# Kernel optimization log

Measured on AMD Instinct MI355X. Metric: run time of the kernel, lower is better.

Reference implementation:

```python
import jax, jax.numpy as jnp
from jax import lax
import numpy as np

B, S, H, L = 128, 256, 768, 24


def setup_inputs() -> dict:
    key = jax.random.key(0)
    k_tf, k_len, k_w, k_tr, k_st, k_en = jax.random.split(key, 6)
    token_features = jax.random.normal(k_tf, (B, S, H), dtype=jnp.float32)
    # contiguous valid lengths in [3, S] (>=3 so that stripping CLS/SEP leaves >=1 token)
    lengths = jax.random.randint(k_len, (B,), 3, S + 1)
    pos = jnp.arange(S)
    input_mask = (pos[None, :] < lengths[:, None]).astype(jnp.int32)
    true_label_mask = (pos[None, :] < (lengths - 2)[:, None]).astype(jnp.int32)
    W = jax.random.normal(k_w, (H, L), dtype=jnp.float32) * 0.02
    b = jnp.zeros((L,), dtype=jnp.float32)
    transitions = jax.random.normal(k_tr, (L, L), dtype=jnp.float32) * 0.1
    start_trans = jax.random.normal(k_st, (L,), dtype=jnp.float32) * 0.1
    end_trans = jax.random.normal(k_en, (L,), dtype=jnp.float32) * 0.1
    return {
        "token_features": token_features,
        "input_mask": input_mask,
        "true_label_mask": true_label_mask,
        "W": W,
        "b": b,
        "transitions": transitions,
        "start_trans": start_trans,
        "end_trans": end_trans,
    }


def _compact(x, mask):
    """Vectorized version of the torch per-token copy loop: for each row,
    gather valid tokens (mask==1) preserving order, drop the first and last
    valid token (CLS/SEP), left-pack into a zero tensor."""
    # stable argsort puts valid positions first, in order
    order = jnp.argsort(1 - mask.astype(jnp.int32), axis=1)  # [B,S]
    gathered = jnp.take_along_axis(x, order[:, :, None], axis=1)  # [B,S,H]
    # drop first valid token (shift left by 1), pad a zero row at the end
    shifted = jnp.concatenate([gathered[:, 1:], jnp.zeros_like(gathered[:, :1])], axis=1)
    n_valid = mask.sum(axis=1)  # [B]
    keep = jnp.arange(x.shape[1])[None, :] < (n_valid[:, None] - 2)  # also drops last (SEP)
    return jnp.where(keep[:, :, None], shifted, 0.0)


def _viterbi(emissions, mask, transitions, start_trans, end_trans):
    """Masked Viterbi decode. emissions [B,S,L], mask [B,S] bool."""
    Bn, Sn, Ln = emissions.shape
    lbl = jnp.arange(Ln)
    score0 = start_trans[None, :] + emissions[:, 0]  # [B,L]

    def step(score, xs):
        em_t, m_t = xs  # [B,L], [B]
        cand = score[:, :, None] + transitions[None]  # [B,prev,curr]
        best = cand.max(axis=1) + em_t
        bp = cand.argmax(axis=1)  # [B,L] best prev tag per curr tag
        new_score = jnp.where(m_t[:, None], best, score)
        bp = jnp.where(m_t[:, None], bp, lbl[None, :])  # identity backpointer on pad
        return new_score, bp

    ems = jnp.swapaxes(emissions[:, 1:], 0, 1)  # [S-1,B,L]
    ms = jnp.swapaxes(mask[:, 1:], 0, 1)  # [S-1,B]
    final, bps = lax.scan(step, score0, (ems, ms))
    final = final + end_trans[None, :]
    best_score = final.max(axis=1)  # [B]
    last_tag = final.argmax(axis=1)  # [B]

    def back(tag, bp):  # tag: tag at time t; bp: bp_t -> tag at t-1
        prev = jnp.take_along_axis(bp, tag[:, None], axis=1)[:, 0]
        return prev, tag

    tag0, tags_rest = lax.scan(back, last_tag, bps, reverse=True)  # tags_rest [S-1,B]
    path = jnp.concatenate([tag0[:, None], jnp.swapaxes(tags_rest, 0, 1)], axis=1)  # [B,S]
    return best_score, path


def reference(token_features, input_mask, true_label_mask, W, b, transitions, start_trans, end_trans):
    mask = input_mask.astype(bool)
    wv = _compact(token_features, mask)  # dropout is identity at inference
    emissions = jax.nn.sigmoid(wv @ W + b)  # [B,S,L]
    _, path = _viterbi(emissions, true_label_mask != 0, transitions, start_trans, end_trans)
    return path
```

## Files before the change

kernel.cpp:

```cpp
#include <hip/hip_runtime.h>
#include <math.h>

#define NB 128
#define NS 256
#define NH 768
#define NL 24
#define ASTR 68
#define SCLS 28

__global__ __launch_bounds__(256) void ner_emis(
    const float* __restrict__ tf, const int* __restrict__ tlm,
    const float* __restrict__ W, const float* __restrict__ bias,
    float* __restrict__ E)
{
    const int b    = blockIdx.x >> 3;
    const int tile = (blockIdx.x & 7) << 5;
    const int tid  = threadIdx.x;
    if (tlm[b*NS + tile] == 0) return;

    __shared__ float lds[8*32*25];
    float* As = lds;
    float* Ws = lds + 32*ASTR;
    float* Pr = lds;

    const int tok  = tid & 15;
    const int ksub = tid >> 4;
    const int kk   = ksub << 2;
    const int rot  = ksub & 3;

    float acc0[NL], acc1[NL];
    #pragma unroll
    for (int l = 0; l < NL; ++l) { acc0[l] = 0.f; acc1[l] = 0.f; }

    const float* tfb = tf + (size_t)(b*NS)*NH;

    const int rowA0 = tid >> 4,            c4A0 = tid & 15;
    const int rowA1 = (tid + 256) >> 4,    c4A1 = tid & 15;
    int trow0 = tile + rowA0 + 1; if (trow0 > 255) trow0 = 255;
    int trow1 = tile + rowA1 + 1; if (trow1 > 255) trow1 = 255;
    const float* srcA0 = tfb + (size_t)trow0*NH + (c4A0 << 2);
    const float* srcA1 = tfb + (size_t)trow1*NH + (c4A1 << 2);

    float4 pa0, pa1, pw0, pw1;
    pa0 = *(const float4*)(srcA0);
    pa1 = *(const float4*)(srcA1);
    {
        const float4* wsrc = (const float4*)(W);
        pw0 = wsrc[tid];
        if (tid < 128) pw1 = wsrc[tid + 256];
    }
    {
        float* d0 = As + rowA0*ASTR + (c4A0 << 2);
        d0[0]=pa0.x; d0[1]=pa0.y; d0[2]=pa0.z; d0[3]=pa0.w;
        float* d1 = As + rowA1*ASTR + (c4A1 << 2);
        d1[0]=pa1.x; d1[1]=pa1.y; d1[2]=pa1.z; d1[3]=pa1.w;
        ((float4*)Ws)[tid] = pw0;
        if (tid < 128) ((float4*)Ws)[tid + 256] = pw1;
    }
    __syncthreads();

    for (int kc0 = 0; kc0 < NH; kc0 += 64) {
        const bool more = (kc0 + 64 < NH);
        if (more) {
            pa0 = *(const float4*)(srcA0 + kc0 + 64);
            pa1 = *(const float4*)(srcA1 + kc0 + 64);
            const float4* wsrc = (const float4*)(W + (size_t)(kc0 + 64)*NL);
            pw0 = wsrc[tid];
            if (tid < 128) pw1 = wsrc[tid + 256];
        }

        const float* A0 = As + tok*ASTR + kk;
        const float* A1 = A0 + 16*ASTR;
        const float* Wr = Ws + kk*NL;
        #pragma unroll
        for (int s = 0; s < 4; ++s) {
            const int j = (s + rot) & 3;
            float a0 = A0[j];
            float a1 = A1[j];
            const float4* w4 = (const float4*)(Wr + j*NL);
            float wv[NL];
            #pragma unroll
            for (int i = 0; i < 6; ++i) {
                float4 w = w4[i];
                wv[4*i+0] = w.x; wv[4*i+1] = w.y; wv[4*i+2] = w.z; wv[4*i+3] = w.w;
            }
            #pragma unroll
            for (int l = 0; l < NL; ++l) {
                acc0[l] = fmaf(a0, wv[l], acc0[l]);
                acc1[l] = fmaf(a1, wv[l], acc1[l]);
            }
        }
        __syncthreads();

        if (more) {
            float* d0 = As + rowA0*ASTR + (c4A0 << 2);
            d0[0]=pa0.x; d0[1]=pa0.y; d0[2]=pa0.z; d0[3]=pa0.w;
            float* d1 = As + rowA1*ASTR + (c4A1 << 2);
            d1[0]=pa1.x; d1[1]=pa1.y; d1[2]=pa1.z; d1[3]=pa1.w;
            ((float4*)Ws)[tid] = pw0;
            if (tid < 128) ((float4*)Ws)[tid + 256] = pw1;
            __syncthreads();
        }
    }

    if (ksub >= 8) {
        float* p = Pr + ((ksub-8)*32 + tok)*25;
        float* q = p + 16*25;
        #pragma unroll
        for (int l = 0; l < NL; ++l) { p[l] = acc0[l]; q[l] = acc1[l]; }
    }
    __syncthreads();
    if (ksub < 8) {
        const float* p = Pr + (ksub*32 + tok)*25;
        const float* q = p + 16*25;
        #pragma unroll
        for (int l = 0; l < NL; ++l) { acc0[l] += p[l]; acc1[l] += q[l]; }
    }
    __syncthreads();
    if (ksub < 8) {
        float* p = Pr + (ksub*32 + tok)*25;
        float* q = p + 16*25;
        #pragma unroll
        for (int l = 0; l < NL; ++l) { p[l] = acc0[l]; q[l] = acc1[l]; }
    }
    __syncthreads();

    const int* tm = tlm + b*NS + tile;
    float* Eb = E + (size_t)(b*NS + tile)*NL;
    #pragma unroll
    for (int i = 0; i < 3; ++i) {
        int o = tid + (i << 8);
        int t = o / NL, l = o % NL;
        if (tm[t]) {
            float s = 0.f;
            #pragma unroll
            for (int ks = 0; ks < 8; ++ks)
                s += Pr[(ks*32 + t)*25 + l];
            float x = s + bias[l];
            Eb[t*NL + l] = 1.0f/(1.0f + expf(-x));
        }
    }
}

__global__ __launch_bounds__(256) void ner_viterbi(
    const float* __restrict__ E, const int* __restrict__ tlm,
    const float* __restrict__ trans, const float* __restrict__ st,
    const float* __restrict__ en, int* __restrict__ out)
{
    const int tid = threadIdx.x;
    const int b   = blockIdx.x;
    const int bS  = b*NS;

    __shared__ float Esh[NS*NL];
    __shared__ float scl[NS*SCLS];
    __shared__ float Tt[NL*NL];
    __shared__ float fin[32];
    __shared__ unsigned char tr_s[NL][NS];
    __shared__ int chosen[12];
    __shared__ int nsh, ltag;

    {
        const float4* src = (const float4*)(E + (size_t)bS*NL);
        float4* dst = (float4*)Esh;
        #pragma unroll
        for (int j = 0; j < 6; ++j) dst[tid + (j << 8)] = src[tid + (j << 8)];
    }
    for (int i = tid; i < NL*NL; i += 256) {
        int c = i / NL, p = i % NL;
        Tt[i] = trans[p*NL + c];
    }
    if (tid < 64) {
        int a = tlm[bS+tid] + tlm[bS+tid+64] + tlm[bS+tid+128] + tlm[bS+tid+192];
        #pragma unroll
        for (int off = 32; off > 0; off >>= 1) a += __shfl_down(a, off, 64);
        if (tid == 0) nsh = a;
    }
    __syncthreads();
    const int n = nsh;

    if (tid < 64) {
        const int lane = tid;
        const int h    = lane >> 5;
        const int c    = lane & 31;
        const int cidx = (c < 24) ? c : 23;
        const int coff = (c < 24) ? c : 24;
        const int p0   = h * 12;

        float Tc[12];
        #pragma unroll
        for (int j = 0; j < 12; ++j) Tc[j] = trans[(p0 + j)*NL + cidx];

        int idxv[12];
        #pragma unroll
        for (int j = 0; j < 12; ++j) idxv[j] = (p0 + j) << 2;

        auto bp = [](int idx4, float v) {
            return __int_as_float(__builtin_amdgcn_ds_bpermute(idx4, __float_as_int(v)));
        };

        float sv = st[cidx] + Esh[cidx];
        scl[coff] = sv;

        auto step = [&](int t, float em) {
            float cand[12];
            #pragma unroll
            for (int j = 0; j < 12; ++j)
                cand[j] = bp(idxv[j], sv) + Tc[j];
            float a0 = fmaxf(fmaxf(cand[0], cand[1]),  cand[2]);
            float a1 = fmaxf(fmaxf(cand[3], cand[4]),  cand[5]);
            float a2 = fmaxf(fmaxf(cand[6], cand[7]),  cand[8]);
            float a3 = fmaxf(fmaxf(cand[9], cand[10]), cand[11]);
            float pm = fmaxf(fmaxf(a0, a1), fmaxf(a2, a3));
#if __has_builtin(__builtin_amdgcn_permlane32_swap)
            auto r = __builtin_amdgcn_permlane32_swap(
                         __float_as_int(pm), __float_as_int(pm), false, false);
            float best = fmaxf(__int_as_float(r[0]), __int_as_float(r[1]));
#else
            float best = fmaxf(pm, bp((lane ^ 32) << 2, pm));
#endif
            sv = best + em;
            scl[t*SCLS + coff] = sv;
        };

        int t = 1;
        for (; t + 8 <= n; t += 8) {
            float em[8];
            const float* eb = Esh + t*NL + cidx;
            #pragma unroll
            for (int j = 0; j < 8; ++j) em[j] = eb[j*NL];
            #pragma unroll
            for (int j = 0; j < 8; ++j) step(t + j, em[j]);
        }
        for (; t < n; ++t) step(t, Esh[t*NL + cidx]);
        fin[c] = sv + en[cidx];
    }
    __syncthreads();

    if (tid == 0) {
        float bv = fin[0]; int bt = 0;
        #pragma unroll
        for (int cc = 1; cc < 24; ++cc) { if (fin[cc] > bv) { bv = fin[cc]; bt = cc; } }
        ltag = bt;
    }
    __syncthreads();

    const int K = (n > 1) ? (n - 1 + 9) / 10 : 1;
    if (n > 1 && tid < 240) {
        const int w = tid / 24 + 1, h = tid % 24;
        int tlo = (w-1)*K; if (tlo > n-1) tlo = n-1;
        int thi = w*K;     if (thi > n-1) thi = n-1;
        int cur = h;
        for (int t = thi; t > tlo; --t) {
            const float4* sp = (const float4*)(scl + (t-1)*SCLS);
            const float4* up = (const float4*)(Tt  + cur*NL);
            float cand[24];
            #pragma unroll
            for (int i = 0; i < 6; ++i) {
                float4 s = sp[i], u = up[i];
                cand[4*i+0] = s.x + u.x;
                cand[4*i+1] = s.y + u.y;
                cand[4*i+2] = s.z + u.z;
                cand[4*i+3] = s.w + u.w;
            }
            float best = cand[0]; int arg = 0;
            #pragma unroll
            for (int p = 1; p < 24; ++p) { if (cand[p] > best) { best = cand[p]; arg = p; } }
            tr_s[h][t-1] = (unsigned char)arg;
            cur = arg;
        }
    }
    __syncthreads();

    if (tid == 0) {
        int cur = ltag;
        for (int w = 10; w >= 1; --w) {
            chosen[w] = cur;
            int tlo = (w-1)*K; if (tlo > n-1) tlo = n-1;
            int thi = w*K;     if (thi > n-1) thi = n-1;
            if (thi > tlo) cur = tr_s[cur][tlo];
        }
    }
    __syncthreads();

    {
        const int t = tid;
        int tag;
        if (t >= n-1) tag = ltag;
        else { int w = t / K + 1; tag = tr_s[chosen[w]][t]; }
        out[bS + t] = tag;
    }
}

extern "C" void kernel_launch(void* const* d_in, const int* in_sizes, int n_in,
                              void* d_out, int out_size, void* d_ws, size_t ws_size,
                              hipStream_t stream) {
    const float* tf    = (const float*)d_in[0];
    const int*   tlm   = (const int*)  d_in[2];
    const float* W     = (const float*)d_in[3];
    const float* bias  = (const float*)d_in[4];
    const float* trans = (const float*)d_in[5];
    const float* st    = (const float*)d_in[6];
    const float* en    = (const float*)d_in[7];
    float* E = (float*)d_ws;

    ner_emis<<<dim3(NB*8), dim3(256), 0, stream>>>(tf, tlm, W, bias, E);
    ner_viterbi<<<dim3(NB), dim3(256), 0, stream>>>(E, tlm, trans, st, en, (int*)d_out);
}
```

Before: 199.9 us.

## Restructure emission GEMM to register-streamed rows and use DPP row-rotate in Viterbi

The emission kernel drops LDS staging of the A and W tiles. Each lane now owns one token and each wave handles a quarter of the K range, reading token features straight from global memory with register prefetch. W is read through uniform scalar loads, and the four wave partials are reduced once in LDS. Blocks grow to 64 tokens, so half as many are launched. The Viterbi recurrence replaces twelve ds_bpermute ops per step with DPP row rotates plus one bpermute swap, masking padded predecessors with a large negative constant. This is meant to cut LDS traffic, barriers and per-step latency, at the cost of more registers and uncoalesced per-lane row loads.

Measured after the change: 298.0 us. 1.49x slower.

```diff
diff --git a/kernel.cpp b/kernel.cpp
--- a/kernel.cpp
+++ b/kernel.cpp
@@ -5,7 +5,6 @@
 #define NS 256
 #define NH 768
 #define NL 24
-#define ASTR 68
 #define SCLS 28
 
 __global__ __launch_bounds__(256) void ner_emis(
@@ -13,131 +12,75 @@
     const float* __restrict__ W, const float* __restrict__ bias,
     float* __restrict__ E)
 {
-    const int b    = blockIdx.x >> 3;
-    const int tile = (blockIdx.x & 7) << 5;
+    const int b    = blockIdx.x >> 2;
+    const int tile = (blockIdx.x & 3) << 6;
     const int tid  = threadIdx.x;
     if (tlm[b*NS + tile] == 0) return;
 
-    __shared__ float lds[8*32*25];
-    float* As = lds;
-    float* Ws = lds + 32*ASTR;
-    float* Pr = lds;
-
-    const int tok  = tid & 15;
-    const int ksub = tid >> 4;
-    const int kk   = ksub << 2;
-    const int rot  = ksub & 3;
-
-    float acc0[NL], acc1[NL];
+    __shared__ float Pr[4*64*25];
+
+    const int lane = tid & 63;
+    const int w    = __builtin_amdgcn_readfirstlane(tid >> 6);
+    const int ks   = w * 192;
+
+    int trow = tile + lane + 1;
+    if (trow > 255) trow = 255;
+    const float* srcA = tf + ((size_t)b*NS + trow)*NH + ks;
+
+    float acc[NL];
     #pragma unroll
-    for (int l = 0; l < NL; ++l) { acc0[l] = 0.f; acc1[l] = 0.f; }
-
-    const float* tfb = tf + (size_t)(b*NS)*NH;
-
-    const int rowA0 = tid >> 4,            c4A0 = tid & 15;
-    const int rowA1 = (tid + 256) >> 4,    c4A1 = tid & 15;
-    int trow0 = tile + rowA0 + 1; if (trow0 > 255) trow0 = 255;
-    int trow1 = tile + rowA1 + 1; if (trow1 > 255) trow1 = 255;
-    const float* srcA0 = tfb + (size_t)trow0*NH + (c4A0 << 2);
-    const float* srcA1 = tfb + (size_t)trow1*NH + (c4A1 << 2);
-
-    float4 pa0, pa1, pw0, pw1;
-    pa0 = *(const float4*)(srcA0);
-    pa1 = *(const float4*)(srcA1);
+    for (int l = 0; l < NL; ++l) acc[l] = 0.f;
+
+    auto fma24 = [&](float av, const float* wr) {
+        #pragma unroll
+        for (int l = 0; l < NL; ++l) acc[l] = fmaf(av, wr[l], acc[l]);
+    };
+
+    float4 c0 = *(const float4*)(srcA);
+    float4 c1 = *(const float4*)(srcA + 4);
+    float4 c2 = *(const float4*)(srcA + 8);
+    float4 c3 = *(const float4*)(srcA + 12);
+
+    for (int kg = 0; kg < 12; ++kg) {
+        float4 n0, n1, n2, n3;
+        const bool more = (kg < 11);
+        if (more) {
+            const float* ns = srcA + ((kg + 1) << 4);
+            n0 = *(const float4*)(ns);
+            n1 = *(const float4*)(ns + 4);
+            n2 = *(const float4*)(ns + 8);
+            n3 = *(const float4*)(ns + 12);
+        }
+        const float* wk = W + (size_t)(ks + (kg << 4))*NL;
+        fma24(c0.x, wk);          fma24(c0.y, wk + NL);
+        fma24(c0.z, wk + 2*NL);   fma24(c0.w, wk + 3*NL);
+        fma24(c1.x, wk + 4*NL);   fma24(c1.y, wk + 5*NL);
+        fma24(c1.z, wk + 6*NL);   fma24(c1.w, wk + 7*NL);
+        fma24(c2.x, wk + 8*NL);   fma24(c2.y, wk + 9*NL);
+        fma24(c2.z, wk + 10*NL);  fma24(c2.w, wk + 11*NL);
+        fma24(c3.x, wk + 12*NL);  fma24(c3.y, wk + 13*NL);
+        fma24(c3.z, wk + 14*NL);  fma24(c3.w, wk + 15*NL);
+        if (more) { c0 = n0; c1 = n1; c2 = n2; c3 = n3; }
+    }
+
     {
-        const float4* wsrc = (const float4*)(W);
-        pw0 = wsrc[tid];
-        if (tid < 128) pw1 = wsrc[tid + 256];
-    }
-    {
-        float* d0 = As + rowA0*ASTR + (c4A0 << 2);
-        d0[0]=pa0.x; d0[1]=pa0.y; d0[2]=pa0.z; d0[3]=pa0.w;
-        float* d1 = As + rowA1*ASTR + (c4A1 << 2);
-        d1[0]=pa1.x; d1[1]=pa1.y; d1[2]=pa1.z; d1[3]=pa1.w;
-        ((float4*)Ws)[tid] = pw0;
-        if (tid < 128) ((float4*)Ws)[tid + 256] = pw1;
-    }
-    __syncthreads();
-
-    for (int kc0 = 0; kc0 < NH; kc0 += 64) {
-        const bool more = (kc0 + 64 < NH);
-        if (more) {
-            pa0 = *(const float4*)(srcA0 + kc0 + 64);
-            pa1 = *(const float4*)(srcA1 + kc0 + 64);
-            const float4* wsrc = (const float4*)(W + (size_t)(kc0 + 64)*NL);
-            pw0 = wsrc[tid];
-            if (tid < 128) pw1 = wsrc[tid + 256];
-        }
-
-        const float* A0 = As + tok*ASTR + kk;
-        const float* A1 = A0 + 16*ASTR;
-        const float* Wr = Ws + kk*NL;
-        #pragma unroll
-        for (int s = 0; s < 4; ++s) {
-            const int j = (s + rot) & 3;
-            float a0 = A0[j];
-            float a1 = A1[j];
-            const float4* w4 = (const float4*)(Wr + j*NL);
-            float wv[NL];
-            #pragma unroll
-            for (int i = 0; i < 6; ++i) {
-                float4 w = w4[i];
-                wv[4*i+0] = w.x; wv[4*i+1] = w.y; wv[4*i+2] = w.z; wv[4*i+3] = w.w;
-            }
-            #pragma unroll
-            for (int l = 0; l < NL; ++l) {
-                acc0[l] = fmaf(a0, wv[l], acc0[l]);
-                acc1[l] = fmaf(a1, wv[l], acc1[l]);
-            }
-        }
-        __syncthreads();
-
-        if (more) {
-            float* d0 = As + rowA0*ASTR + (c4A0 << 2);
-            d0[0]=pa0.x; d0[1]=pa0.y; d0[2]=pa0.z; d0[3]=pa0.w;
-            float* d1 = As + rowA1*ASTR + (c4A1 << 2);
-            d1[0]=pa1.x; d1[1]=pa1.y; d1[2]=pa1.z; d1[3]=pa1.w;
-            ((float4*)Ws)[tid] = pw0;
-            if (tid < 128) ((float4*)Ws)[tid + 256] = pw1;
-            __syncthreads();
-        }
-    }
-
-    if (ksub >= 8) {
-        float* p = Pr + ((ksub-8)*32 + tok)*25;
-        float* q = p + 16*25;
-        #pragma unroll
-        for (int l = 0; l < NL; ++l) { p[l] = acc0[l]; q[l] = acc1[l]; }
-    }
-    __syncthreads();
-    if (ksub < 8) {
-        const float* p = Pr + (ksub*32 + tok)*25;
-        const float* q = p + 16*25;
-        #pragma unroll
-        for (int l = 0; l < NL; ++l) { acc0[l] += p[l]; acc1[l] += q[l]; }
-    }
-    __syncthreads();
-    if (ksub < 8) {
-        float* p = Pr + (ksub*32 + tok)*25;
-        float* q = p + 16*25;
-        #pragma unroll
-        for (int l = 0; l < NL; ++l) { p[l] = acc0[l]; q[l] = acc1[l]; }
+        float* p = Pr + ((w << 6) + lane)*25;
+        #pragma unroll
+        for (int l = 0; l < NL; ++l) p[l] = acc[l];
     }
     __syncthreads();
 
     const int* tm = tlm + b*NS + tile;
     float* Eb = E + (size_t)(b*NS + tile)*NL;
     #pragma unroll
-    for (int i = 0; i < 3; ++i) {
+    for (int i = 0; i < 6; ++i) {
         int o = tid + (i << 8);
-        int t = o / NL, l = o % NL;
+        int t = o / NL, l = o - t*NL;
         if (tm[t]) {
-            float s = 0.f;
-            #pragma unroll
-            for (int ks = 0; ks < 8; ++ks)
-                s += Pr[(ks*32 + t)*25 + l];
+            float s = ((Pr[t*25 + l] + Pr[(64 + t)*25 + l])
+                       + Pr[(128 + t)*25 + l]) + Pr[(192 + t)*25 + l];
             float x = s + bias[l];
-            Eb[t*NL + l] = 1.0f/(1.0f + expf(-x));
+            Eb[o] = 1.0f/(1.0f + expf(-x));
         }
     }
 }
@@ -180,45 +123,55 @@
 
     if (tid < 64) {
         const int lane = tid;
-        const int h    = lane >> 5;
         const int c    = lane & 31;
         const int cidx = (c < 24) ? c : 23;
         const int coff = (c < 24) ? c : 24;
-        const int p0   = h * 12;
-
-        float Tc[12];
-        #pragma unroll
-        for (int j = 0; j < 12; ++j) Tc[j] = trans[(p0 + j)*NL + cidx];
-
-        int idxv[12];
-        #pragma unroll
-        for (int j = 0; j < 12; ++j) idxv[j] = (p0 + j) << 2;
-
-        auto bp = [](int idx4, float v) {
-            return __int_as_float(__builtin_amdgcn_ds_bpermute(idx4, __float_as_int(v)));
-        };
+        const int swIdx = (lane ^ 16) << 2;
+
+        float TA[16], TB[16];
+        {
+            int aP = c;
+            int bP = (lane ^ 16) & 31;
+            TA[0] = (c < 24 && aP < 24) ? trans[aP*NL + cidx] : -1e30f;
+            TB[0] = (c < 24 && bP < 24) ? trans[bP*NL + cidx] : -1e30f;
+        }
+        #define CAL(r) { \
+            int srcl = __builtin_amdgcn_update_dpp(lane, lane, (0x120 + r), 0xF, 0xF, false); \
+            int aP = srcl & 31; int bP = (srcl ^ 16) & 31; \
+            TA[r] = (c < 24 && aP < 24) ? trans[aP*NL + cidx] : -1e30f; \
+            TB[r] = (c < 24 && bP < 24) ? trans[bP*NL + cidx] : -1e30f; }
+        CAL(1)  CAL(2)  CAL(3)  CAL(4)  CAL(5)  CAL(6)  CAL(7)
+        CAL(8)  CAL(9)  CAL(10) CAL(11) CAL(12) CAL(13) CAL(14) CAL(15)
+        #undef CAL
 
         float sv = st[cidx] + Esh[cidx];
         scl[coff] = sv;
 
+        #define F3(x,y,z) fmaxf(fmaxf(x,y),z)
+
         auto step = [&](int t, float em) {
-            float cand[12];
-            #pragma unroll
-            for (int j = 0; j < 12; ++j)
-                cand[j] = bp(idxv[j], sv) + Tc[j];
-            float a0 = fmaxf(fmaxf(cand[0], cand[1]),  cand[2]);
-            float a1 = fmaxf(fmaxf(cand[3], cand[4]),  cand[5]);
-            float a2 = fmaxf(fmaxf(cand[6], cand[7]),  cand[8]);
-            float a3 = fmaxf(fmaxf(cand[9], cand[10]), cand[11]);
-            float pm = fmaxf(fmaxf(a0, a1), fmaxf(a2, a3));
-#if __has_builtin(__builtin_amdgcn_permlane32_swap)
-            auto r = __builtin_amdgcn_permlane32_swap(
-                         __float_as_int(pm), __float_as_int(pm), false, false);
-            float best = fmaxf(__int_as_float(r[0]), __int_as_float(r[1]));
-#else
-            float best = fmaxf(pm, bp((lane ^ 32) << 2, pm));
-#endif
-            sv = best + em;
+            int svi = __float_as_int(sv);
+            int swi = __builtin_amdgcn_ds_bpermute(swIdx, svi);
+            float aa0 = sv + TA[0];
+            #define CA(r) float aa##r = __int_as_float(__builtin_amdgcn_update_dpp( \
+                svi, svi, (0x120 + r), 0xF, 0xF, false)) + TA[r];
+            CA(1)  CA(2)  CA(3)  CA(4)  CA(5)  CA(6)  CA(7)
+            CA(8)  CA(9)  CA(10) CA(11) CA(12) CA(13) CA(14) CA(15)
+            #undef CA
+            float mA = fmaxf(fmaxf(F3(aa0,aa1,aa2),  F3(aa3,aa4,aa5)),
+                       fmaxf(F3(aa6,aa7,aa8),
+                       fmaxf(F3(aa9,aa10,aa11), fmaxf(F3(aa12,aa13,aa14), aa15))));
+            float sswap = __int_as_float(swi);
+            float bb0 = sswap + TB[0];
+            #define CB(r) float bb##r = __int_as_float(__builtin_amdgcn_update_dpp( \
+                swi, swi, (0x120 + r), 0xF, 0xF, false)) + TB[r];
+            CB(1)  CB(2)  CB(3)  CB(4)  CB(5)  CB(6)  CB(7)
+            CB(8)  CB(9)  CB(10) CB(11) CB(12) CB(13) CB(14) CB(15)
+            #undef CB
+            float mB = fmaxf(fmaxf(F3(bb0,bb1,bb2),  F3(bb3,bb4,bb5)),
+                       fmaxf(F3(bb6,bb7,bb8),
+                       fmaxf(F3(bb9,bb10,bb11), fmaxf(F3(bb12,bb13,bb14), bb15))));
+            sv = fmaxf(mA, mB) + em;
             scl[t*SCLS + coff] = sv;
         };
 
@@ -303,6 +256,6 @@
     const float* en    = (const float*)d_in[7];
     float* E = (float*)d_ws;
 
-    ner_emis<<<dim3(NB*8), dim3(256), 0, stream>>>(tf, tlm, W, bias, E);
+    ner_emis<<<dim3(NB*4), dim3(256), 0, stream>>>(tf, tlm, W, bias, E);
     ner_viterbi<<<dim3(NB), dim3(256), 0, stream>>>(E, tlm, trans, st, en, (int*)d_out);
 }
```

## Fuse emission GEMM and Viterbi into one kernel with per-tile flag handoff

Applied to the files above, without the earlier changes.

Merges the emission projection kernel and the Viterbi kernel into a single launch. The first NB blocks run Viterbi and spin on per-tile release flags written by the emission blocks, so each decode chunk starts as soon as its 32-token tile is ready instead of waiting for a full kernel boundary. Emissions are read directly from global memory in 32-step chunks rather than staged into LDS. This removes the launch gap and lets the Viterbi recursion overlap with the GEMM. The cost is an extra memset launch and spinning blocks that hold compute units, and forward progress depends on the emission blocks being scheduled while the Viterbi blocks wait.

After: 252.1 us. +26.1%, slower.

```diff
diff --git a/kernel.cpp b/kernel.cpp
--- a/kernel.cpp
+++ b/kernel.cpp
@@ -7,176 +7,178 @@
 #define NL 24
 #define ASTR 68
 #define SCLS 28
-
-__global__ __launch_bounds__(256) void ner_emis(
+#define E_BYTES (NB*NS*NL*4)
+
+__global__ __launch_bounds__(256) void ner_fused(
     const float* __restrict__ tf, const int* __restrict__ tlm,
     const float* __restrict__ W, const float* __restrict__ bias,
-    float* __restrict__ E)
+    const float* __restrict__ trans, const float* __restrict__ st,
+    const float* __restrict__ en, float* __restrict__ E,
+    int* __restrict__ flags, int* __restrict__ out)
 {
-    const int b    = blockIdx.x >> 3;
-    const int tile = (blockIdx.x & 7) << 5;
-    const int tid  = threadIdx.x;
-    if (tlm[b*NS + tile] == 0) return;
-
-    __shared__ float lds[8*32*25];
-    float* As = lds;
-    float* Ws = lds + 32*ASTR;
-    float* Pr = lds;
-
-    const int tok  = tid & 15;
-    const int ksub = tid >> 4;
-    const int kk   = ksub << 2;
-    const int rot  = ksub & 3;
-
-    float acc0[NL], acc1[NL];
-    #pragma unroll
-    for (int l = 0; l < NL; ++l) { acc0[l] = 0.f; acc1[l] = 0.f; }
-
-    const float* tfb = tf + (size_t)(b*NS)*NH;
-
-    const int rowA0 = tid >> 4,            c4A0 = tid & 15;
-    const int rowA1 = (tid + 256) >> 4,    c4A1 = tid & 15;
-    int trow0 = tile + rowA0 + 1; if (trow0 > 255) trow0 = 255;
-    int trow1 = tile + rowA1 + 1; if (trow1 > 255) trow1 = 255;
-    const float* srcA0 = tfb + (size_t)trow0*NH + (c4A0 << 2);
-    const float* srcA1 = tfb + (size_t)trow1*NH + (c4A1 << 2);
-
-    float4 pa0, pa1, pw0, pw1;
-    pa0 = *(const float4*)(srcA0);
-    pa1 = *(const float4*)(srcA1);
-    {
-        const float4* wsrc = (const float4*)(W);
-        pw0 = wsrc[tid];
-        if (tid < 128) pw1 = wsrc[tid + 256];
-    }
-    {
-        float* d0 = As + rowA0*ASTR + (c4A0 << 2);
-        d0[0]=pa0.x; d0[1]=pa0.y; d0[2]=pa0.z; d0[3]=pa0.w;
-        float* d1 = As + rowA1*ASTR + (c4A1 << 2);
-        d1[0]=pa1.x; d1[1]=pa1.y; d1[2]=pa1.z; d1[3]=pa1.w;
-        ((float4*)Ws)[tid] = pw0;
-        if (tid < 128) ((float4*)Ws)[tid + 256] = pw1;
-    }
-    __syncthreads();
-
-    for (int kc0 = 0; kc0 < NH; kc0 += 64) {
-        const bool more = (kc0 + 64 < NH);
-        if (more) {
-            pa0 = *(const float4*)(srcA0 + kc0 + 64);
-            pa1 = *(const float4*)(srcA1 + kc0 + 64);
-            const float4* wsrc = (const float4*)(W + (size_t)(kc0 + 64)*NL);
+    __shared__ __align__(16) unsigned char smem[37376];
+    const int tid = threadIdx.x;
+
+    if (blockIdx.x >= NB) {
+        const int bid  = blockIdx.x - NB;
+        const int b    = bid >> 3;
+        const int tile = (bid & 7) << 5;
+        if (tlm[b*NS + tile] == 0) {
+            if (tid == 0)
+                __hip_atomic_store(flags + bid, 1, __ATOMIC_RELEASE, __HIP_MEMORY_SCOPE_AGENT);
+            return;
+        }
+
+        float* lds = (float*)smem;
+        float* As = lds;
+        float* Ws = lds + 32*ASTR;
+        float* Pr = lds;
+
+        const int tok  = tid & 15;
+        const int ksub = tid >> 4;
+        const int kk   = ksub << 2;
+        const int rot  = ksub & 3;
+
+        float acc0[NL], acc1[NL];
+        #pragma unroll
+        for (int l = 0; l < NL; ++l) { acc0[l] = 0.f; acc1[l] = 0.f; }
+
+        const float* tfb = tf + (size_t)(b*NS)*NH;
+
+        const int rowA0 = tid >> 4,         c4A0 = tid & 15;
+        const int rowA1 = (tid + 256) >> 4, c4A1 = tid & 15;
+        int trow0 = tile + rowA0 + 1; if (trow0 > 255) trow0 = 255;
+        int trow1 = tile + rowA1 + 1; if (trow1 > 255) trow1 = 255;
+        const float* srcA0 = tfb + (size_t)trow0*NH + (c4A0 << 2);
+        const float* srcA1 = tfb + (size_t)trow1*NH + (c4A1 << 2);
+
+        float4 pa0, pa1, pw0, pw1;
+        pa0 = *(const float4*)(srcA0);
+        pa1 = *(const float4*)(srcA1);
+        {
+            const float4* wsrc = (const float4*)(W);
             pw0 = wsrc[tid];
             if (tid < 128) pw1 = wsrc[tid + 256];
         }
-
-        const float* A0 = As + tok*ASTR + kk;
-        const float* A1 = A0 + 16*ASTR;
-        const float* Wr = Ws + kk*NL;
-        #pragma unroll
-        for (int s = 0; s < 4; ++s) {
-            const int j = (s + rot) & 3;
-            float a0 = A0[j];
-            float a1 = A1[j];
-            const float4* w4 = (const float4*)(Wr + j*NL);
-            float wv[NL];
-            #pragma unroll
-            for (int i = 0; i < 6; ++i) {
-                float4 w = w4[i];
-                wv[4*i+0] = w.x; wv[4*i+1] = w.y; wv[4*i+2] = w.z; wv[4*i+3] = w.w;
-            }
-            #pragma unroll
-            for (int l = 0; l < NL; ++l) {
-                acc0[l] = fmaf(a0, wv[l], acc0[l]);
-                acc1[l] = fmaf(a1, wv[l], acc1[l]);
-            }
-        }
-        __syncthreads();
-
-        if (more) {
+        {
             float* d0 = As + rowA0*ASTR + (c4A0 << 2);
             d0[0]=pa0.x; d0[1]=pa0.y; d0[2]=pa0.z; d0[3]=pa0.w;
             float* d1 = As + rowA1*ASTR + (c4A1 << 2);
             d1[0]=pa1.x; d1[1]=pa1.y; d1[2]=pa1.z; d1[3]=pa1.w;
             ((float4*)Ws)[tid] = pw0;
             if (tid < 128) ((float4*)Ws)[tid + 256] = pw1;
+        }
+        __syncthreads();
+
+        for (int kc0 = 0; kc0 < NH; kc0 += 64) {
+            const bool more = (kc0 + 64 < NH);
+            if (more) {
+                pa0 = *(const float4*)(srcA0 + kc0 + 64);
+                pa1 = *(const float4*)(srcA1 + kc0 + 64);
+                const float4* wsrc = (const float4*)(W + (size_t)(kc0 + 64)*NL);
+                pw0 = wsrc[tid];
+                if (tid < 128) pw1 = wsrc[tid + 256];
+            }
+
+            const float* A0 = As + tok*ASTR + kk;
+            const float* A1 = A0 + 16*ASTR;
+            const float* Wr = Ws + kk*NL;
+            #pragma unroll
+            for (int s = 0; s < 4; ++s) {
+                const int j = (s + rot) & 3;
+                float a0 = A0[j];
+                float a1 = A1[j];
+                const float4* w4 = (const float4*)(Wr + j*NL);
+                float wv[NL];
+                #pragma unroll
+                for (int i = 0; i < 6; ++i) {
+                    float4 w = w4[i];
+                    wv[4*i+0] = w.x; wv[4*i+1] = w.y; wv[4*i+2] = w.z; wv[4*i+3] = w.w;
+                }
+                #pragma unroll
+                for (int l = 0; l < NL; ++l) {
+                    acc0[l] = fmaf(a0, wv[l], acc0[l]);
+                    acc1[l] = fmaf(a1, wv[l], acc1[l]);
+                }
+            }
             __syncthreads();
-        }
-    }
-
-    if (ksub >= 8) {
-        float* p = Pr + ((ksub-8)*32 + tok)*25;
-        float* q = p + 16*25;
-        #pragma unroll
-        for (int l = 0; l < NL; ++l) { p[l] = acc0[l]; q[l] = acc1[l]; }
-    }
-    __syncthreads();
-    if (ksub < 8) {
-        const float* p = Pr + (ksub*32 + tok)*25;
-        const float* q = p + 16*25;
-        #pragma unroll
-        for (int l = 0; l < NL; ++l) { acc0[l] += p[l]; acc1[l] += q[l]; }
-    }
-    __syncthreads();
-    if (ksub < 8) {
-        float* p = Pr + (ksub*32 + tok)*25;
-        float* q = p + 16*25;
-        #pragma unroll
-        for (int l = 0; l < NL; ++l) { p[l] = acc0[l]; q[l] = acc1[l]; }
-    }
-    __syncthreads();
-
-    const int* tm = tlm + b*NS + tile;
-    float* Eb = E + (size_t)(b*NS + tile)*NL;
-    #pragma unroll
-    for (int i = 0; i < 3; ++i) {
-        int o = tid + (i << 8);
-        int t = o / NL, l = o % NL;
-        if (tm[t]) {
-            float s = 0.f;
-            #pragma unroll
-            for (int ks = 0; ks < 8; ++ks)
-                s += Pr[(ks*32 + t)*25 + l];
-            float x = s + bias[l];
-            Eb[t*NL + l] = 1.0f/(1.0f + expf(-x));
-        }
-    }
-}
-
-__global__ __launch_bounds__(256) void ner_viterbi(
-    const float* __restrict__ E, const int* __restrict__ tlm,
-    const float* __restrict__ trans, const float* __restrict__ st,
-    const float* __restrict__ en, int* __restrict__ out)
-{
-    const int tid = threadIdx.x;
-    const int b   = blockIdx.x;
-    const int bS  = b*NS;
-
-    __shared__ float Esh[NS*NL];
-    __shared__ float scl[NS*SCLS];
-    __shared__ float Tt[NL*NL];
-    __shared__ float fin[32];
-    __shared__ unsigned char tr_s[NL][NS];
-    __shared__ int chosen[12];
-    __shared__ int nsh, ltag;
-
-    {
-        const float4* src = (const float4*)(E + (size_t)bS*NL);
-        float4* dst = (float4*)Esh;
-        #pragma unroll
-        for (int j = 0; j < 6; ++j) dst[tid + (j << 8)] = src[tid + (j << 8)];
-    }
+
+            if (more) {
+                float* d0 = As + rowA0*ASTR + (c4A0 << 2);
+                d0[0]=pa0.x; d0[1]=pa0.y; d0[2]=pa0.z; d0[3]=pa0.w;
+                float* d1 = As + rowA1*ASTR + (c4A1 << 2);
+                d1[0]=pa1.x; d1[1]=pa1.y; d1[2]=pa1.z; d1[3]=pa1.w;
+                ((float4*)Ws)[tid] = pw0;
+                if (tid < 128) ((float4*)Ws)[tid + 256] = pw1;
+                __syncthreads();
+            }
+        }
+
+        if (ksub >= 8) {
+            float* p = Pr + ((ksub-8)*32 + tok)*25;
+            float* q = p + 16*25;
+            #pragma unroll
+            for (int l = 0; l < NL; ++l) { p[l] = acc0[l]; q[l] = acc1[l]; }
+        }
+        __syncthreads();
+        if (ksub < 8) {
+            const float* p = Pr + (ksub*32 + tok)*25;
+            const float* q = p + 16*25;
+            #pragma unroll
+            for (int l = 0; l < NL; ++l) { acc0[l] += p[l]; acc1[l] += q[l]; }
+        }
+        __syncthreads();
+        if (ksub < 8) {
+            float* p = Pr + (ksub*32 + tok)*25;
+            float* q = p + 16*25;
+            #pragma unroll
+            for (int l = 0; l < NL; ++l) { p[l] = acc0[l]; q[l] = acc1[l]; }
+        }
+        __syncthreads();
+
+        const int* tm = tlm + b*NS + tile;
+        float* Eb = E + (size_t)(b*NS + tile)*NL;
+        #pragma unroll
+        for (int i = 0; i < 3; ++i) {
+            int o = tid + (i << 8);
+            int t = o / NL, l = o % NL;
+            if (tm[t]) {
+                float s = 0.f;
+                #pragma unroll
+                for (int ks = 0; ks < 8; ++ks)
+                    s += Pr[(ks*32 + t)*25 + l];
+                float x = s + bias[l];
+                Eb[t*NL + l] = 1.0f/(1.0f + expf(-x));
+            }
+        }
+        __syncthreads();
+        if (tid == 0)
+            __hip_atomic_store(flags + bid, 1, __ATOMIC_RELEASE, __HIP_MEMORY_SCOPE_AGENT);
+        return;
+    }
+
+    const int b  = blockIdx.x;
+    const int bS = b*NS;
+
+    float* scl = (float*)smem;
+    float* Tt  = (float*)(smem + 28672);
+    float* fin = (float*)(smem + 30976);
+    int*   chosen = (int*)(smem + 31104);
+    int*   misc   = (int*)(smem + 31152);
+    unsigned char* tr_s = smem + 31160;
+
     for (int i = tid; i < NL*NL; i += 256) {
-        int c = i / NL, p = i % NL;
-        Tt[i] = trans[p*NL + c];
+        int cc = i / NL, p = i % NL;
+        Tt[i] = trans[p*NL + cc];
     }
     if (tid < 64) {
         int a = tlm[bS+tid] + tlm[bS+tid+64] + tlm[bS+tid+128] + tlm[bS+tid+192];
         #pragma unroll
         for (int off = 32; off > 0; off >>= 1) a += __shfl_down(a, off, 64);
-        if (tid == 0) nsh = a;
-    }
-    __syncthreads();
-    const int n = nsh;
+        if (tid == 0) misc[0] = a;
+    }
+    __syncthreads();
+    const int n = misc[0];
 
     if (tid < 64) {
         const int lane = tid;
@@ -198,8 +200,9 @@
             return __int_as_float(__builtin_amdgcn_ds_bpermute(idx4, __float_as_int(v)));
         };
 
-        float sv = st[cidx] + Esh[cidx];
-        scl[coff] = sv;
+        const float* Eg = E + (size_t)bS*NL + cidx;
+        int* fl = flags + b*8;
+        float sv = 0.f;
 
         auto step = [&](int t, float em) {
             float cand[12];
@@ -222,16 +225,27 @@
             scl[t*SCLS + coff] = sv;
         };
 
-        int t = 1;
-        for (; t + 8 <= n; t += 8) {
-            float em[8];
-            const float* eb = Esh + t*NL + cidx;
-            #pragma unroll
-            for (int j = 0; j < 8; ++j) em[j] = eb[j*NL];
-            #pragma unroll
-            for (int j = 0; j < 8; ++j) step(t + j, em[j]);
-        }
-        for (; t < n; ++t) step(t, Esh[t*NL + cidx]);
+        const int jmax = (n - 1) >> 5;
+        for (int jt = 0; jt <= jmax; ++jt) {
+            while (__hip_atomic_load(fl + jt, __ATOMIC_RELAXED, __HIP_MEMORY_SCOPE_AGENT) == 0)
+                __builtin_amdgcn_s_sleep(2);
+            __threadfence();
+
+            float em[32];
+            #pragma unroll
+            for (int i = 0; i < 32; ++i)
+                em[i] = Eg[(size_t)((jt << 5) + i)*NL];
+
+            if (jt == 0) {
+                sv = st[cidx] + em[0];
+                scl[coff] = sv;
+            }
+            #pragma unroll
+            for (int i = 0; i < 32; ++i) {
+                const int t = (jt << 5) + i;
+                if (t >= 1 && t < n) step(t, em[i]);
+            }
+        }
         fin[c] = sv + en[cidx];
     }
     __syncthreads();
@@ -240,9 +254,10 @@
         float bv = fin[0]; int bt = 0;
         #pragma unroll
         for (int cc = 1; cc < 24; ++cc) { if (fin[cc] > bv) { bv = fin[cc]; bt = cc; } }
-        ltag = bt;
-    }
-    __syncthreads();
+        misc[1] = bt;
+    }
+    __syncthreads();
+    const int ltag = misc[1];
 
     const int K = (n > 1) ? (n - 1 + 9) / 10 : 1;
     if (n > 1 && tid < 240) {
@@ -265,7 +280,7 @@
             float best = cand[0]; int arg = 0;
             #pragma unroll
             for (int p = 1; p < 24; ++p) { if (cand[p] > best) { best = cand[p]; arg = p; } }
-            tr_s[h][t-1] = (unsigned char)arg;
+            tr_s[h*NS + (t-1)] = (unsigned char)arg;
             cur = arg;
         }
     }
@@ -277,7 +292,7 @@
             chosen[w] = cur;
             int tlo = (w-1)*K; if (tlo > n-1) tlo = n-1;
             int thi = w*K;     if (thi > n-1) thi = n-1;
-            if (thi > tlo) cur = tr_s[cur][tlo];
+            if (thi > tlo) cur = tr_s[cur*NS + tlo];
         }
     }
     __syncthreads();
@@ -286,7 +301,7 @@
         const int t = tid;
         int tag;
         if (t >= n-1) tag = ltag;
-        else { int w = t / K + 1; tag = tr_s[chosen[w]][t]; }
+        else { int w = t / K + 1; tag = tr_s[chosen[w]*NS + t]; }
         out[bS + t] = tag;
     }
 }
@@ -301,8 +316,10 @@
     const float* trans = (const float*)d_in[5];
     const float* st    = (const float*)d_in[6];
     const float* en    = (const float*)d_in[7];
-    float* E = (float*)d_ws;
-
-    ner_emis<<<dim3(NB*8), dim3(256), 0, stream>>>(tf, tlm, W, bias, E);
-    ner_viterbi<<<dim3(NB), dim3(256), 0, stream>>>(E, tlm, trans, st, en, (int*)d_out);
+    float* E     = (float*)d_ws;
+    int*   flags = (int*)((char*)d_ws + E_BYTES);
+
+    hipMemsetAsync(flags, 0, NB*8*sizeof(int), stream);
+    ner_fused<<<dim3(NB + NB*8), dim3(256), 0, stream>>>(
+        tf, tlm, W, bias, trans, st, en, E, flags, (int*)d_out);
 }
```
